# Kernel tuning notes

Measured on AMD Instinct MI355X. Metric: run time of the kernel, lower is better.

## Reference

```python
import jax, jax.numpy as jnp
import numpy as np

N = 50000
NEG_SLOPE = 0.2


def gat_conv(x, src, dst, W, al, ar, b, res=None, activation=None):
    # x: [N, F_in]; W: [F_in, H*D]; al, ar: [H, D]; b: [H*D]
    H, D = al.shape
    h = (x @ W).reshape(-1, H, D)                      # [N, H, D]
    el = jnp.sum(h * al, axis=-1)                      # [N, H]
    er = jnp.sum(h * ar, axis=-1)                      # [N, H]
    e = jax.nn.leaky_relu(el[src] + er[dst], NEG_SLOPE)  # [E, H]
    # edge softmax grouped by destination node
    m = jax.ops.segment_max(e, dst, num_segments=N)    # [N, H]
    ex = jnp.exp(e - m[dst])
    s = jax.ops.segment_sum(ex, dst, num_segments=N)   # [N, H]
    alpha = ex / s[dst]                                # [E, H]
    msg = h[src] * alpha[..., None]                    # [E, H, D]
    out = jax.ops.segment_sum(msg, dst, num_segments=N)  # [N, H, D]
    if res is not None:
        if res is True:  # identity residual (F_in == H*D)
            out = out + x.reshape(-1, H, D)
        else:            # projected residual, res: [F_in, H*D]
            out = out + (x @ res).reshape(-1, H, D)
    out = out + b.reshape(1, H, D)
    if activation is not None:
        out = activation(out)
    return out


def setup_inputs() -> dict:
    key = jax.random.key(0)
    ks = jax.random.split(key, 16)
    E = 800000
    IN, HID, CLS, H = 256, 64, 32, 2
    x = jax.random.normal(ks[0], (N, IN), dtype=jnp.float32)
    edge_src = jax.random.randint(ks[1], (E,), 0, N, dtype=jnp.int32)
    edge_dst = jax.random.randint(ks[2], (E,), 0, N, dtype=jnp.int32)

    def lin(k, fi, fo):
        return jax.random.normal(k, (fi, fo), dtype=jnp.float32) * (1.0 / np.sqrt(fi))

    W0 = lin(ks[3], IN, H * HID)
    al0 = jax.random.normal(ks[4], (H, HID), dtype=jnp.float32) * 0.1
    ar0 = jax.random.normal(ks[5], (H, HID), dtype=jnp.float32) * 0.1
    b0 = jnp.zeros((H * HID,), dtype=jnp.float32)
    W1 = lin(ks[6], H * HID, H * HID)
    al1 = jax.random.normal(ks[7], (H, HID), dtype=jnp.float32) * 0.1
    ar1 = jax.random.normal(ks[8], (H, HID), dtype=jnp.float32) * 0.1
    b1 = jnp.zeros((H * HID,), dtype=jnp.float32)
    W2 = lin(ks[9], H * HID, H * CLS)
    al2 = jax.random.normal(ks[10], (H, CLS), dtype=jnp.float32) * 0.1
    ar2 = jax.random.normal(ks[11], (H, CLS), dtype=jnp.float32) * 0.1
    b2 = jnp.zeros((H * CLS,), dtype=jnp.float32)
    Wres2 = lin(ks[12], H * HID, H * CLS)
    return {"x": x, "edge_src": edge_src, "edge_dst": edge_dst,
            "W0": W0, "al0": al0, "ar0": ar0, "b0": b0,
            "W1": W1, "al1": al1, "ar1": ar1, "b1": b1,
            "W2": W2, "al2": al2, "ar2": ar2, "b2": b2,
            "Wres2": Wres2}


def reference(x, edge_src, edge_dst, W0, al0, ar0, b0, W1, al1, ar1, b1,
              W2, al2, ar2, b2, Wres2):
    elu = jax.nn.elu
    h = gat_conv(x, edge_src, edge_dst, W0, al0, ar0, b0,
                 res=None, activation=elu)
    h = h.reshape(h.shape[0], -1)  # flatten heads: [N, H*D]
    h = gat_conv(h, edge_src, edge_dst, W1, al1, ar1, b1,
                 res=True, activation=elu)  # identity residual
    h = h.reshape(h.shape[0], -1)
    h = gat_conv(h, edge_src, edge_dst, W2, al2, ar2, b2,
                 res=Wres2, activation=None)  # [N, H, CLS]
    logits = h.mean(axis=1)  # mean over heads -> [N, CLS]
    return logits
```

## Files before the change

### kernel.cpp

```cpp
#include <hip/hip_runtime.h>
#include <math.h>


typedef unsigned int uint;
typedef unsigned short ushort;
typedef __attribute__((ext_vector_type(8))) short bf16x8;
typedef __attribute__((ext_vector_type(4))) float f32x4;

#define NBK 196
#define BCAP 4608

__device__ inline uint f2bf(float f) {
    uint u = __float_as_uint(f);
    return (u + 0x7fffu + ((u >> 16) & 1u)) >> 16;
}

__device__ inline uint4 pack8(float4 a, float4 b) {
    return make_uint4(f2bf(a.x) | (f2bf(a.y) << 16), f2bf(a.z) | (f2bf(a.w) << 16),
                      f2bf(b.x) | (f2bf(b.y) << 16), f2bf(b.z) | (f2bf(b.w) << 16));
}

__global__ __launch_bounds__(256) void bucketA_k(
    const int* __restrict__ src, const int* __restrict__ dst, int E,
    int* __restrict__ bcur, uint* __restrict__ bdata) {
    __shared__ int lhist[NBK];
    __shared__ int gbase[NBK];
    const int t = threadIdx.x;
    for (int i = t; i < NBK; i += 256) lhist[i] = 0;
    __syncthreads();
    const int e0 = blockIdx.x * 2048 + t * 8;
    uint payload[8], meta[8];
#pragma unroll
    for (int i = 0; i < 8; ++i) {
        int e = e0 + i;
        if (e < E) {
            int s = src[e], d = dst[e];
            int b = d >> 8;
            int r = atomicAdd(&lhist[b], 1);
            payload[i] = ((uint)s << 8) | (uint)(d & 255);
            meta[i] = ((uint)b << 16) | (uint)r;
        } else {
            meta[i] = 0xffffffffu;
        }
    }
    __syncthreads();
    for (int i = t; i < NBK; i += 256) {
        int c = lhist[i];
        gbase[i] = c ? atomicAdd(&bcur[i], c) : 0;
    }
    __syncthreads();
#pragma unroll
    for (int i = 0; i < 8; ++i) {
        if (meta[i] != 0xffffffffu) {
            int b = meta[i] >> 16;
            int pos = gbase[b] + (int)(meta[i] & 0xffffu);
            if (pos < BCAP) bdata[(size_t)b * BCAP + pos] = payload[i];
        }
    }
}

__global__ __launch_bounds__(256) void bscan_k(const int* __restrict__ bcur,
                                               int* __restrict__ bbase) {
    __shared__ int sm[256];
    int t = threadIdx.x;
    int v = (t < NBK) ? min(bcur[t], BCAP) : 0;
    sm[t] = v;
    __syncthreads();
    for (int o = 1; o < 256; o <<= 1) {
        int add = (t >= o) ? sm[t - o] : 0;
        __syncthreads();
        sm[t] += add;
        __syncthreads();
    }
    if (t < NBK) bbase[t] = sm[t] - v;
}

__global__ __launch_bounds__(256) void bucketB_k(
    const uint* __restrict__ bdata, const int* __restrict__ bcur,
    const int* __restrict__ bbase, int* __restrict__ deg,
    int* __restrict__ offs, int* __restrict__ ssrc, int n) {
    __shared__ int lhist[256], lofs[256], lcur[256], stmp[256];
    const int b = blockIdx.x, t = threadIdx.x;
    const int cnt = min(bcur[b], BCAP);
    const int gb = bbase[b];
    lhist[t] = 0;
    __syncthreads();
    const uint* bd = bdata + (size_t)b * BCAP;
    for (int i = t; i < cnt; i += 256)
        atomicAdd(&lhist[bd[i] & 255], 1);
    __syncthreads();
    int v = lhist[t];
    stmp[t] = v;
    __syncthreads();
    for (int o = 1; o < 256; o <<= 1) {
        int add = (t >= o) ? stmp[t - o] : 0;
        __syncthreads();
        stmp[t] += add;
        __syncthreads();
    }
    lofs[t] = stmp[t] - v;
    lcur[t] = 0;
    __syncthreads();
    int node = b * 256 + t;
    if (node < n) {
        deg[node] = v;
        offs[node] = gb + lofs[t];
    }
    for (int i = t; i < cnt; i += 256) {
        uint p = bd[i];
        int dl = p & 255;
        int r = atomicAdd(&lcur[dl], 1);
        ssrc[gb + lofs[dl] + r] = (int)(p >> 8);
    }
}

__global__ __launch_bounds__(256) void wt_k(
    const float* __restrict__ W0, const float* __restrict__ W1,
    const float* __restrict__ W2, const float* __restrict__ Wr,
    ushort* __restrict__ Wt0, ushort* __restrict__ Wt1,
    ushort* __restrict__ Wt2cat) {
    int b = blockIdx.x, t = threadIdx.x;
    if (b < 128) {
        int i = b * 256 + t;
        int n = i >> 8, k = i & 255;
        Wt0[n * 256 + k] = (ushort)f2bf(W0[k * 128 + n]);
    } else if (b < 192) {
        int i = (b - 128) * 256 + t;
        int n = i >> 7, k = i & 127;
        Wt1[n * 128 + k] = (ushort)f2bf(W1[k * 128 + n]);
    } else if (b < 224) {
        int i = (b - 192) * 256 + t;
        int n = i >> 7, k = i & 127;
        Wt2cat[n * 128 + k] = (ushort)f2bf(W2[k * 64 + n]);
    } else {
        int i = (b - 224) * 256 + t;
        int n = i >> 7, k = i & 127;
        Wt2cat[(64 + n) * 128 + k] = (ushort)f2bf(Wr[k * 64 + n]);
    }
}

template <int K, bool L2MODE, bool AFP32>
__global__ __launch_bounds__(256) void gemm_m(
    const float* __restrict__ Af, const ushort* __restrict__ Ab,
    const ushort* __restrict__ Wt, ushort* __restrict__ Hb,
    float* __restrict__ hres, int nrows,
    const float* __restrict__ al, const float* __restrict__ ar,
    float* __restrict__ el, float* __restrict__ er) {
    constexpr int BK = 64;
    constexpr int AS = 72;
    __shared__ float smem[8448 + 256];
    ushort* As = (ushort*)smem;
    ushort* Ws = (ushort*)smem + 64 * AS;
    float* alr = smem + 8448;
    const int tid = threadIdx.x;
    const int w = tid >> 6;
    const int lane = tid & 63;
    const int l15 = lane & 15, quad = lane >> 4;
    const int row0 = blockIdx.x * 64;
    constexpr int NC = L2MODE ? 64 : 128;

    if (tid < 2 * NC) alr[tid] = (tid < NC) ? al[tid] : ar[tid - NC];

    f32x4 acc[8];
#pragma unroll
    for (int i = 0; i < 8; ++i) acc[i] = (f32x4){0.f, 0.f, 0.f, 0.f};

    for (int kt = 0; kt < K / BK; ++kt) {
        const int k0 = kt * BK;
        if (AFP32) {
#pragma unroll
            for (int t = 0; t < 4; ++t) {
                int idx = tid + t * 256;
                int r = idx >> 4, c4 = idx & 15;
                float4 v = make_float4(0.f, 0.f, 0.f, 0.f);
                if (row0 + r < nrows)
                    v = *(const float4*)&Af[(size_t)(row0 + r) * K + k0 + c4 * 4];
                ushort4 o;
                o.x = (ushort)f2bf(v.x); o.y = (ushort)f2bf(v.y);
                o.z = (ushort)f2bf(v.z); o.w = (ushort)f2bf(v.w);
                *(ushort4*)&As[r * AS + c4 * 4] = o;
            }
        } else {
#pragma unroll
            for (int t = 0; t < 2; ++t) {
                int idx = tid + t * 256;
                int r = idx >> 3, c8 = idx & 7;
                uint4 v = make_uint4(0, 0, 0, 0);
                if (row0 + r < nrows)
                    v = *(const uint4*)&Ab[(size_t)(row0 + r) * K + k0 + c8 * 8];
                *(uint4*)&As[r * AS + c8 * 8] = v;
            }
        }
#pragma unroll
        for (int t = 0; t < 4; ++t) {
            int idx = tid + t * 256;
            int n = idx >> 3, c8 = idx & 7;
            *(uint4*)&Ws[n * AS + c8 * 8] =
                *(const uint4*)&Wt[(size_t)n * K + k0 + c8 * 8];
        }
        __syncthreads();
#pragma unroll
        for (int ks = 0; ks < 2; ++ks) {
            bf16x8 af = *(const bf16x8*)&As[(w * 16 + l15) * AS + ks * 32 + quad * 8];
#pragma unroll
            for (int ct = 0; ct < 8; ++ct) {
                bf16x8 bf = *(const bf16x8*)&Ws[(ct * 16 + l15) * AS + ks * 32 + quad * 8];
                acc[ct] = __builtin_amdgcn_mfma_f32_16x16x32_bf16(af, bf, acc[ct], 0, 0, 0);
            }
        }
        __syncthreads();
    }

    float* Cs = smem;
#pragma unroll
    for (int ct = 0; ct < 8; ++ct)
#pragma unroll
        for (int r = 0; r < 4; ++r)
            Cs[(w * 16 + quad * 4 + r) * 132 + ct * 16 + l15] = acc[ct][r];
    __syncthreads();

    if (L2MODE) {
#pragma unroll
        for (int t = 0; t < 2; ++t) {
            int chunk = tid + t * 256;
            int r = chunk >> 3, c8 = chunk & 7;
            int grow = row0 + r;
            if (grow < nrows) {
                float4 v0 = *(float4*)&Cs[r * 132 + c8 * 8];
                float4 v1 = *(float4*)&Cs[r * 132 + c8 * 8 + 4];
                *(uint4*)&Hb[(size_t)grow * 64 + c8 * 8] = pack8(v0, v1);
            }
        }
#pragma unroll
        for (int t = 0; t < 4; ++t) {
            int chunk = tid + t * 256;
            int r = chunk >> 4, c4 = chunk & 15;
            int grow = row0 + r;
            if (grow < nrows)
                *(float4*)&hres[(size_t)grow * 64 + c4 * 4] =
                    *(float4*)&Cs[r * 132 + 64 + c4 * 4];
        }
    } else {
#pragma unroll
        for (int t = 0; t < 4; ++t) {
            int chunk = tid + t * 256;
            int r = chunk >> 4, c8 = chunk & 15;
            int grow = row0 + r;
            if (grow < nrows) {
                float4 v0 = *(float4*)&Cs[r * 132 + c8 * 8];
                float4 v1 = *(float4*)&Cs[r * 132 + c8 * 8 + 4];
                *(uint4*)&Hb[(size_t)grow * 128 + c8 * 8] = pack8(v0, v1);
            }
        }
    }
    {
        constexpr int HD = L2MODE ? 32 : 64;
        int r = tid >> 2, hh = (tid >> 1) & 1, iser = tid & 1;
        int grow = row0 + r;
        const float* coef = alr + iser * NC + hh * HD;
        const float* crow = Cs + r * 132 + hh * HD;
        float sum = 0.f;
#pragma unroll
        for (int i = 0; i < HD; ++i) sum += crow[i] * coef[i];
        if (grow < nrows) (iser ? er : el)[grow * 2 + hh] = sum;
    }
}

template <int D, bool MEAN_HEADS, bool RES_BF16>
__global__ __launch_bounds__(256) void agg_c(
    const int* __restrict__ ssrc, const int* __restrict__ offs,
    const int* __restrict__ deg, const ushort* __restrict__ hb,
    const float* __restrict__ el, const float* __restrict__ er,
    const float* __restrict__ bias, const void* __restrict__ res,
    float* __restrict__ out, ushort* __restrict__ outb, int act, int n) {
    constexpr int F = 2 * D;
    constexpr int CH = F / 8;
    constexpr int ES = 64 / CH;
    constexpr int UB = 4;
    __shared__ float2 wls_all[4][128];
    const int wid = threadIdx.x >> 6;
    const int lane = threadIdx.x & 63;
    const int node = blockIdx.x * 4 + wid;
    if (node >= n) return;
    float2* wls = wls_all[wid];
    const int off = offs[node];
    const int dg = deg[node];
    const float2 ern = *(const float2*)&er[node * 2];

    float m0, m1, is0, is1;
    const bool small = (dg <= 64);
    if (small) {
        int sidx = 0;
        float a = -INFINITY, b = -INFINITY;
        if (lane < dg) {
            sidx = ssrc[off + lane];
            float2 ev = *(const float2*)&el[sidx * 2];
            a = ev.x + ern.x; a = fmaxf(a, 0.2f * a);
            b = ev.y + ern.y; b = fmaxf(b, 0.2f * b);
        }
        m0 = a; m1 = b;
        for (int o = 32; o; o >>= 1) {
            m0 = fmaxf(m0, __shfl_xor(m0, o));
            m1 = fmaxf(m1, __shfl_xor(m1, o));
        }
        float p0 = (lane < dg) ? __expf(a - m0) : 0.f;
        float p1 = (lane < dg) ? __expf(b - m1) : 0.f;
        float s0 = p0, s1 = p1;
        for (int o = 32; o; o >>= 1) {
            s0 += __shfl_xor(s0, o);
            s1 += __shfl_xor(s1, o);
        }
        is0 = s0 > 0.f ? 1.f / s0 : 0.f;
        is1 = s1 > 0.f ? 1.f / s1 : 0.f;
        wls[lane * 2 + 0] = make_float2(__int_as_float(sidx), p0 * is0);
        wls[lane * 2 + 1] = make_float2(__int_as_float(sidx), p1 * is1);
    } else {
        float s0 = 0.f, s1 = 0.f;
        m0 = -INFINITY; m1 = -INFINITY;
        for (int k = lane; k < dg; k += 64) {
            int sidx = ssrc[off + k];
            float2 ev = *(const float2*)&el[sidx * 2];
            float a = ev.x + ern.x; a = fmaxf(a, 0.2f * a);
            float b = ev.y + ern.y; b = fmaxf(b, 0.2f * b);
            float nm = fmaxf(m0, a);
            s0 = s0 * __expf(m0 - nm) + __expf(a - nm); m0 = nm;
            nm = fmaxf(m1, b);
            s1 = s1 * __expf(m1 - nm) + __expf(b - nm); m1 = nm;
        }
        for (int o = 32; o; o >>= 1) {
            float om = __shfl_xor(m0, o), os = __shfl_xor(s0, o);
            float nm = fmaxf(m0, om);
            s0 = (nm == -INFINITY) ? 0.f : s0 * __expf(m0 - nm) + os * __expf(om - nm);
            m0 = nm;
            om = __shfl_xor(m1, o); os = __shfl_xor(s1, o);
            nm = fmaxf(m1, om);
            s1 = (nm == -INFINITY) ? 0.f : s1 * __expf(m1 - nm) + os * __expf(om - nm);
            m1 = nm;
        }
        is0 = s0 > 0.f ? 1.f / s0 : 0.f;
        is1 = s1 > 0.f ? 1.f / s1 : 0.f;
    }

    const int c = lane & (CH - 1);
    const int es = lane / CH;
    const int h1 = (c >= CH / 2) ? 1 : 0;
    const uint4* __restrict__ hp = (const uint4*)hb;
    const float2* wbase = wls + es * 2 + h1;
    float acc[8];
#pragma unroll
    for (int i = 0; i < 8; ++i) acc[i] = 0.f;

    for (int c0 = 0; c0 < dg; c0 += 64) {
        if (!small) {
            int k = c0 + lane;
            int sidx = 0;
            float w0 = 0.f, w1 = 0.f;
            if (k < dg) {
                sidx = ssrc[off + k];
                float2 ev = *(const float2*)&el[sidx * 2];
                float a = ev.x + ern.x; a = fmaxf(a, 0.2f * a);
                float b = ev.y + ern.y; b = fmaxf(b, 0.2f * b);
                w0 = __expf(a - m0) * is0;
                w1 = __expf(b - m1) * is1;
            }
            wls[lane * 2 + 0] = make_float2(__int_as_float(sidx), w0);
            wls[lane * 2 + 1] = make_float2(__int_as_float(sidx), w1);
        }
        const int cnt = min(64, dg - c0);
        for (int p = 0; p < cnt; p += UB * ES) {
            float2 mw[UB];
#pragma unroll
            for (int u = 0; u < UB; ++u)
                mw[u] = wbase[(p + u * ES) * 2];
            uint4 q[UB];
#pragma unroll
            for (int u = 0; u < UB; ++u)
                q[u] = hp[(size_t)__float_as_int(mw[u].x) * CH + c];
#pragma unroll
            for (int u = 0; u < UB; ++u) {
                float wj = mw[u].y;
                acc[0] += wj * __uint_as_float(q[u].x << 16);
                acc[1] += wj * __uint_as_float(q[u].x & 0xffff0000u);
                acc[2] += wj * __uint_as_float(q[u].y << 16);
                acc[3] += wj * __uint_as_float(q[u].y & 0xffff0000u);
                acc[4] += wj * __uint_as_float(q[u].z << 16);
                acc[5] += wj * __uint_as_float(q[u].z & 0xffff0000u);
                acc[6] += wj * __uint_as_float(q[u].w << 16);
                acc[7] += wj * __uint_as_float(q[u].w & 0xffff0000u);
            }
        }
    }

#pragma unroll
    for (int o = CH; o < 64; o <<= 1) {
#pragma unroll
        for (int i = 0; i < 8; ++i) acc[i] += __shfl_xor(acc[i], o);
    }

    const int f0 = c * 8;
    float4 b0v = *(const float4*)&bias[f0];
    float4 b1v = *(const float4*)&bias[f0 + 4];
    float vv[8] = {acc[0] + b0v.x, acc[1] + b0v.y, acc[2] + b0v.z, acc[3] + b0v.w,
                   acc[4] + b1v.x, acc[5] + b1v.y, acc[6] + b1v.z, acc[7] + b1v.w};
    if (res) {
        if (RES_BF16) {
            uint4 r = ((const uint4*)res)[(size_t)node * CH + c];
            vv[0] += __uint_as_float(r.x << 16);
            vv[1] += __uint_as_float(r.x & 0xffff0000u);
            vv[2] += __uint_as_float(r.y << 16);
            vv[3] += __uint_as_float(r.y & 0xffff0000u);
            vv[4] += __uint_as_float(r.z << 16);
            vv[5] += __uint_as_float(r.z & 0xffff0000u);
            vv[6] += __uint_as_float(r.w << 16);
            vv[7] += __uint_as_float(r.w & 0xffff0000u);
        } else {
            const float* rf = (const float*)res;
            float4 r0v = *(const float4*)&rf[(size_t)node * F + f0];
            float4 r1v = *(const float4*)&rf[(size_t)node * F + f0 + 4];
            vv[0] += r0v.x; vv[1] += r0v.y; vv[2] += r0v.z; vv[3] += r0v.w;
            vv[4] += r1v.x; vv[5] += r1v.y; vv[6] += r1v.z; vv[7] += r1v.w;
        }
    }
    if (act) {
#pragma unroll
        for (int i = 0; i < 8; ++i)
            vv[i] = vv[i] > 0.f ? vv[i] : __expf(vv[i]) - 1.f;
    }
    if (MEAN_HEADS) {
        float ov[8];
#pragma unroll
        for (int i = 0; i < 8; ++i) ov[i] = __shfl_xor(vv[i], CH / 2);
        if (es == 0 && c < CH / 2) {
            float4 u0 = make_float4(0.5f * (vv[0] + ov[0]), 0.5f * (vv[1] + ov[1]),
                                    0.5f * (vv[2] + ov[2]), 0.5f * (vv[3] + ov[3]));
            float4 u1 = make_float4(0.5f * (vv[4] + ov[4]), 0.5f * (vv[5] + ov[5]),
                                    0.5f * (vv[6] + ov[6]), 0.5f * (vv[7] + ov[7]));
            *(float4*)&out[(size_t)node * D + f0] = u0;
            *(float4*)&out[(size_t)node * D + f0 + 4] = u1;
        }
    } else if (es == 0) {
        if (out) {
            *(float4*)&out[(size_t)node * F + f0] =
                make_float4(vv[0], vv[1], vv[2], vv[3]);
            *(float4*)&out[(size_t)node * F + f0 + 4] =
                make_float4(vv[4], vv[5], vv[6], vv[7]);
        }
        if (outb) {
            *(uint4*)&outb[(size_t)node * F + f0] =
                pack8(make_float4(vv[0], vv[1], vv[2], vv[3]),
                      make_float4(vv[4], vv[5], vv[6], vv[7]));
        }
    }
}


extern "C" void kernel_launch(void* const* d_in, const int* in_sizes, int n_in,
                              void* d_out, int out_size, void* d_ws, size_t ws_size,
                              hipStream_t stream) {
    const float* x     = (const float*)d_in[0];
    const int*   esrc  = (const int*)d_in[1];
    const int*   edst  = (const int*)d_in[2];
    const float* W0    = (const float*)d_in[3];
    const float* al0   = (const float*)d_in[4];
    const float* ar0   = (const float*)d_in[5];
    const float* b0    = (const float*)d_in[6];
    const float* W1    = (const float*)d_in[7];
    const float* al1   = (const float*)d_in[8];
    const float* ar1   = (const float*)d_in[9];
    const float* b1    = (const float*)d_in[10];
    const float* W2    = (const float*)d_in[11];
    const float* al2   = (const float*)d_in[12];
    const float* ar2   = (const float*)d_in[13];
    const float* b2    = (const float*)d_in[14];
    const float* Wres2 = (const float*)d_in[15];

    const int N = in_sizes[0] / 256;
    const int E = in_sizes[1];

    float* ws = (float*)d_ws;
    float* hres  = ws;
    float* el    = hres + (size_t)N * 64;
    float* er    = el + (size_t)N * 2;
    int* deg     = (int*)(er + (size_t)N * 2);
    int* offs    = deg + N;
    int* bcur    = offs + N;
    int* bbase   = bcur + 256;
    int* ssrc    = bbase + 256;
    uint* bdata  = (uint*)(ssrc + E);
    ushort* Hb   = (ushort*)(bdata + (size_t)NBK * BCAP);
    ushort* Ab   = Hb + (size_t)N * 128;
    ushort* Bb   = Ab + (size_t)N * 128;
    ushort* Wt0  = Bb + (size_t)N * 128;
    ushort* Wt1  = Wt0 + 128 * 256;
    ushort* Wt2c = Wt1 + 128 * 128;

    hipMemsetAsync(bcur, 0, NBK * sizeof(int), stream);
    bucketA_k<<<(E + 2047) / 2048, 256, 0, stream>>>(esrc, edst, E, bcur, bdata);
    bscan_k<<<1, 256, 0, stream>>>(bcur, bbase);
    bucketB_k<<<NBK, 256, 0, stream>>>(bdata, bcur, bbase, deg, offs, ssrc, N);

    wt_k<<<256, 256, 0, stream>>>(W0, W1, W2, Wres2, Wt0, Wt1, Wt2c);

    int gblk = (N + 63) / 64;
    int ablk = (N + 3) / 4;

    gemm_m<256, false, true><<<gblk, 256, 0, stream>>>(
        x, nullptr, Wt0, Hb, nullptr, N, al0, ar0, el, er);
    agg_c<64, false, false><<<ablk, 256, 0, stream>>>(
        ssrc, offs, deg, Hb, el, er, b0, nullptr, nullptr, Ab, 1, N);

    gemm_m<128, false, false><<<gblk, 256, 0, stream>>>(
        nullptr, Ab, Wt1, Hb, nullptr, N, al1, ar1, el, er);
    agg_c<64, false, true><<<ablk, 256, 0, stream>>>(
        ssrc, offs, deg, Hb, el, er, b1, Ab, nullptr, Bb, 1, N);

    gemm_m<128, true, false><<<gblk, 256, 0, stream>>>(
        nullptr, Bb, Wt2c, Hb, hres, N, al2, ar2, el, er);
    agg_c<32, true, false><<<ablk, 256, 0, stream>>>(
        ssrc, offs, deg, Hb, el, er, b2, hres, (float*)d_out, nullptr, 0, N);
}
```

Before: 305.0 us.

## Bin nodes by degree and pack several low-degree nodes per wavefront

Adds a binning pass that sorts nodes into three degree classes (≤16, ≤32, >32) and a persistent aggregation kernel that processes 4, 2 or 1 nodes per 64-lane wavefront depending on class. With average degree around 16, most wavefronts previously left many lanes idle during the softmax and gather phases. The cost is two extra small kernels, a memset, and indirection through node lists, which also change the output write order. The node lists reuse the bucket scratch buffer, which is no longer needed at that point.

```diff
diff --git a/kernel.cpp b/kernel.cpp
--- a/kernel.cpp
+++ b/kernel.cpp
@@ -112,6 +112,37 @@
         int r = atomicAdd(&lcur[dl], 1);
         ssrc[gb + lofs[dl] + r] = (int)(p >> 8);
     }
+}
+
+__global__ __launch_bounds__(256) void bin_k(
+    const int* __restrict__ deg, int n, int* __restrict__ nl0,
+    int* __restrict__ nl1, int* __restrict__ nl2, int* __restrict__ cnt) {
+    __shared__ int lc[3], lb[3];
+    const int t = threadIdx.x;
+    if (t < 3) lc[t] = 0;
+    __syncthreads();
+    int node = blockIdx.x * 256 + t;
+    int cls = -1, r = 0;
+    if (node < n) {
+        int d = deg[node];
+        cls = (d <= 16) ? 0 : ((d <= 32) ? 1 : 2);
+        r = atomicAdd(&lc[cls], 1);
+    }
+    __syncthreads();
+    if (t < 3) lb[t] = lc[t] ? atomicAdd(&cnt[t], lc[t]) : 0;
+    __syncthreads();
+    if (node < n) {
+        int* nl = (cls == 0) ? nl0 : ((cls == 1) ? nl1 : nl2);
+        nl[lb[cls] + r] = node;
+    }
+}
+
+__global__ void sched_k(int* __restrict__ meta) {
+    int I0 = (meta[0] + 3) >> 2;
+    int I1 = (meta[1] + 1) >> 1;
+    meta[3] = I0;
+    meta[4] = I0 + I1;
+    meta[5] = I0 + I1 + meta[2];
 }
 
 __global__ __launch_bounds__(256) void wt_k(
@@ -266,112 +297,43 @@
     }
 }
 
-template <int D, bool MEAN_HEADS, bool RES_BF16>
-__global__ __launch_bounds__(256) void agg_c(
+template <int D, bool MEAN_HEADS, bool RES_BF16, int LPN>
+__device__ __forceinline__ void agg_group(
+    int node, int lane, float2* __restrict__ wlsw,
     const int* __restrict__ ssrc, const int* __restrict__ offs,
     const int* __restrict__ deg, const ushort* __restrict__ hb,
     const float* __restrict__ el, const float* __restrict__ er,
     const float* __restrict__ bias, const void* __restrict__ res,
-    float* __restrict__ out, ushort* __restrict__ outb, int act, int n) {
+    float* __restrict__ out, ushort* __restrict__ outb, int act) {
     constexpr int F = 2 * D;
     constexpr int CH = F / 8;
-    constexpr int ES = 64 / CH;
+    constexpr int ESL = LPN / CH;
     constexpr int UB = 4;
-    __shared__ float2 wls_all[4][128];
-    const int wid = threadIdx.x >> 6;
-    const int lane = threadIdx.x & 63;
-    const int node = blockIdx.x * 4 + wid;
-    if (node >= n) return;
-    float2* wls = wls_all[wid];
-    const int off = offs[node];
-    const int dg = deg[node];
-    const float2 ern = *(const float2*)&er[node * 2];
-
-    float m0, m1, is0, is1;
-    const bool small = (dg <= 64);
-    if (small) {
-        int sidx = 0;
-        float a = -INFINITY, b = -INFINITY;
-        if (lane < dg) {
-            sidx = ssrc[off + lane];
-            float2 ev = *(const float2*)&el[sidx * 2];
-            a = ev.x + ern.x; a = fmaxf(a, 0.2f * a);
-            b = ev.y + ern.y; b = fmaxf(b, 0.2f * b);
-        }
-        m0 = a; m1 = b;
-        for (int o = 32; o; o >>= 1) {
-            m0 = fmaxf(m0, __shfl_xor(m0, o));
-            m1 = fmaxf(m1, __shfl_xor(m1, o));
-        }
-        float p0 = (lane < dg) ? __expf(a - m0) : 0.f;
-        float p1 = (lane < dg) ? __expf(b - m1) : 0.f;
-        float s0 = p0, s1 = p1;
-        for (int o = 32; o; o >>= 1) {
-            s0 += __shfl_xor(s0, o);
-            s1 += __shfl_xor(s1, o);
-        }
-        is0 = s0 > 0.f ? 1.f / s0 : 0.f;
-        is1 = s1 > 0.f ? 1.f / s1 : 0.f;
-        wls[lane * 2 + 0] = make_float2(__int_as_float(sidx), p0 * is0);
-        wls[lane * 2 + 1] = make_float2(__int_as_float(sidx), p1 * is1);
-    } else {
-        float s0 = 0.f, s1 = 0.f;
-        m0 = -INFINITY; m1 = -INFINITY;
-        for (int k = lane; k < dg; k += 64) {
-            int sidx = ssrc[off + k];
-            float2 ev = *(const float2*)&el[sidx * 2];
-            float a = ev.x + ern.x; a = fmaxf(a, 0.2f * a);
-            float b = ev.y + ern.y; b = fmaxf(b, 0.2f * b);
-            float nm = fmaxf(m0, a);
-            s0 = s0 * __expf(m0 - nm) + __expf(a - nm); m0 = nm;
-            nm = fmaxf(m1, b);
-            s1 = s1 * __expf(m1 - nm) + __expf(b - nm); m1 = nm;
-        }
-        for (int o = 32; o; o >>= 1) {
-            float om = __shfl_xor(m0, o), os = __shfl_xor(s0, o);
-            float nm = fmaxf(m0, om);
-            s0 = (nm == -INFINITY) ? 0.f : s0 * __expf(m0 - nm) + os * __expf(om - nm);
-            m0 = nm;
-            om = __shfl_xor(m1, o); os = __shfl_xor(s1, o);
-            nm = fmaxf(m1, om);
-            s1 = (nm == -INFINITY) ? 0.f : s1 * __expf(m1 - nm) + os * __expf(om - nm);
-            m1 = nm;
-        }
-        is0 = s0 > 0.f ? 1.f / s0 : 0.f;
-        is1 = s1 > 0.f ? 1.f / s1 : 0.f;
-    }
-
-    const int c = lane & (CH - 1);
-    const int es = lane / CH;
+    static_assert(ESL >= 1, "LPN must cover a full row");
+    const int g = lane / LPN, sl = lane % LPN;
+    const bool valid = node >= 0;
+    float2* wls = wlsw + g * (LPN * 2);
+    int off = 0, dg = 0;
+    float2 ern = make_float2(0.f, 0.f);
+    if (valid) {
+        off = offs[node];
+        dg = deg[node];
+        ern = *(const float2*)&er[node * 2];
+    }
+    const uint4* __restrict__ hp = (const uint4*)hb;
+    const int c = sl & (CH - 1);
+    const int es = sl / CH;
     const int h1 = (c >= CH / 2) ? 1 : 0;
-    const uint4* __restrict__ hp = (const uint4*)hb;
     const float2* wbase = wls + es * 2 + h1;
     float acc[8];
 #pragma unroll
     for (int i = 0; i < 8; ++i) acc[i] = 0.f;
 
-    for (int c0 = 0; c0 < dg; c0 += 64) {
-        if (!small) {
-            int k = c0 + lane;
-            int sidx = 0;
-            float w0 = 0.f, w1 = 0.f;
-            if (k < dg) {
-                sidx = ssrc[off + k];
-                float2 ev = *(const float2*)&el[sidx * 2];
-                float a = ev.x + ern.x; a = fmaxf(a, 0.2f * a);
-                float b = ev.y + ern.y; b = fmaxf(b, 0.2f * b);
-                w0 = __expf(a - m0) * is0;
-                w1 = __expf(b - m1) * is1;
-            }
-            wls[lane * 2 + 0] = make_float2(__int_as_float(sidx), w0);
-            wls[lane * 2 + 1] = make_float2(__int_as_float(sidx), w1);
-        }
-        const int cnt = min(64, dg - c0);
-        for (int p = 0; p < cnt; p += UB * ES) {
+    auto inner = [&](int cnt) {
+        for (int p = 0; p < cnt; p += UB * ESL) {
             float2 mw[UB];
 #pragma unroll
-            for (int u = 0; u < UB; ++u)
-                mw[u] = wbase[(p + u * ES) * 2];
+            for (int u = 0; u < UB; ++u) mw[u] = wbase[(p + u * ESL) * 2];
             uint4 q[UB];
 #pragma unroll
             for (int u = 0; u < UB; ++u)
@@ -389,13 +351,88 @@
                 acc[7] += wj * __uint_as_float(q[u].w & 0xffff0000u);
             }
         }
-    }
-
-#pragma unroll
-    for (int o = CH; o < 64; o <<= 1) {
+    };
+
+    bool big = false;
+    if constexpr (LPN == 64) big = (dg > 64);
+
+    if (!big) {
+        int sidx = 0;
+        float a = -INFINITY, b = -INFINITY;
+        if (valid && sl < dg) {
+            sidx = ssrc[off + sl];
+            float2 ev = *(const float2*)&el[sidx * 2];
+            a = ev.x + ern.x; a = fmaxf(a, 0.2f * a);
+            b = ev.y + ern.y; b = fmaxf(b, 0.2f * b);
+        }
+        float m0 = a, m1 = b;
+#pragma unroll
+        for (int o = LPN / 2; o; o >>= 1) {
+            m0 = fmaxf(m0, __shfl_xor(m0, o));
+            m1 = fmaxf(m1, __shfl_xor(m1, o));
+        }
+        float p0 = (valid && sl < dg) ? __expf(a - m0) : 0.f;
+        float p1 = (valid && sl < dg) ? __expf(b - m1) : 0.f;
+        float s0 = p0, s1 = p1;
+#pragma unroll
+        for (int o = LPN / 2; o; o >>= 1) {
+            s0 += __shfl_xor(s0, o);
+            s1 += __shfl_xor(s1, o);
+        }
+        float is0 = s0 > 0.f ? 1.f / s0 : 0.f;
+        float is1 = s1 > 0.f ? 1.f / s1 : 0.f;
+        wls[sl * 2 + 0] = make_float2(__int_as_float(sidx), p0 * is0);
+        wls[sl * 2 + 1] = make_float2(__int_as_float(sidx), p1 * is1);
+        inner(dg);
+    } else if constexpr (LPN == 64) {
+        float s0 = 0.f, s1 = 0.f;
+        float m0 = -INFINITY, m1 = -INFINITY;
+        for (int k = sl; k < dg; k += 64) {
+            int sidx = ssrc[off + k];
+            float2 ev = *(const float2*)&el[sidx * 2];
+            float a = ev.x + ern.x; a = fmaxf(a, 0.2f * a);
+            float b = ev.y + ern.y; b = fmaxf(b, 0.2f * b);
+            float nm = fmaxf(m0, a);
+            s0 = s0 * __expf(m0 - nm) + __expf(a - nm); m0 = nm;
+            nm = fmaxf(m1, b);
+            s1 = s1 * __expf(m1 - nm) + __expf(b - nm); m1 = nm;
+        }
+        for (int o = 32; o; o >>= 1) {
+            float om = __shfl_xor(m0, o), os = __shfl_xor(s0, o);
+            float nm = fmaxf(m0, om);
+            s0 = (nm == -INFINITY) ? 0.f : s0 * __expf(m0 - nm) + os * __expf(om - nm);
+            m0 = nm;
+            om = __shfl_xor(m1, o); os = __shfl_xor(s1, o);
+            nm = fmaxf(m1, om);
+            s1 = (nm == -INFINITY) ? 0.f : s1 * __expf(m1 - nm) + os * __expf(om - nm);
+            m1 = nm;
+        }
+        float is0 = s0 > 0.f ? 1.f / s0 : 0.f;
+        float is1 = s1 > 0.f ? 1.f / s1 : 0.f;
+        for (int cc = 0; cc < dg; cc += 64) {
+            int k = cc + sl;
+            int sidx = 0;
+            float w0 = 0.f, w1 = 0.f;
+            if (k < dg) {
+                sidx = ssrc[off + k];
+                float2 ev = *(const float2*)&el[sidx * 2];
+                float a = ev.x + ern.x; a = fmaxf(a, 0.2f * a);
+                float b = ev.y + ern.y; b = fmaxf(b, 0.2f * b);
+                w0 = __expf(a - m0) * is0;
+                w1 = __expf(b - m1) * is1;
+            }
+            wls[sl * 2 + 0] = make_float2(__int_as_float(sidx), w0);
+            wls[sl * 2 + 1] = make_float2(__int_as_float(sidx), w1);
+            inner(min(64, dg - cc));
+        }
+    }
+
+#pragma unroll
+    for (int o = CH; o < LPN; o <<= 1) {
 #pragma unroll
         for (int i = 0; i < 8; ++i) acc[i] += __shfl_xor(acc[i], o);
     }
+    if (!valid) return;
 
     const int f0 = c * 8;
     float4 b0v = *(const float4*)&bias[f0];
@@ -453,6 +490,44 @@
     }
 }
 
+template <int D, bool MEAN_HEADS, bool RES_BF16>
+__global__ __launch_bounds__(256) void agg_c2(
+    const int* __restrict__ meta, const int* __restrict__ nl0,
+    const int* __restrict__ nl1, const int* __restrict__ nl2,
+    const int* __restrict__ ssrc, const int* __restrict__ offs,
+    const int* __restrict__ deg, const ushort* __restrict__ hb,
+    const float* __restrict__ el, const float* __restrict__ er,
+    const float* __restrict__ bias, const void* __restrict__ res,
+    float* __restrict__ out, ushort* __restrict__ outb, int act) {
+    __shared__ float2 wls_all[4][128];
+    const int wid = threadIdx.x >> 6;
+    const int lane = threadIdx.x & 63;
+    float2* wls = wls_all[wid];
+    const int c0 = meta[0], c1 = meta[1];
+    const int I0 = meta[3], I01 = meta[4], T = meta[5];
+    const int nW = gridDim.x * 4;
+    for (int it = blockIdx.x * 4 + wid; it < T; it += nW) {
+        if (it < I0) {
+            int idx = it * 4 + (lane >> 4);
+            int node = (idx < c0) ? nl0[idx] : -1;
+            agg_group<D, MEAN_HEADS, RES_BF16, 16>(node, lane, wls, ssrc, offs,
+                                                   deg, hb, el, er, bias, res,
+                                                   out, outb, act);
+        } else if (it < I01) {
+            int idx = (it - I0) * 2 + (lane >> 5);
+            int node = (idx < c1) ? nl1[idx] : -1;
+            agg_group<D, MEAN_HEADS, RES_BF16, 32>(node, lane, wls, ssrc, offs,
+                                                   deg, hb, el, er, bias, res,
+                                                   out, outb, act);
+        } else {
+            int node = nl2[it - I01];
+            agg_group<D, MEAN_HEADS, RES_BF16, 64>(node, lane, wls, ssrc, offs,
+                                                   deg, hb, el, er, bias, res,
+                                                   out, outb, act);
+        }
+    }
+}
+
 
 extern "C" void kernel_launch(void* const* d_in, const int* in_sizes, int n_in,
                               void* d_out, int out_size, void* d_ws, size_t ws_size,
@@ -494,28 +569,40 @@
     ushort* Wt1  = Wt0 + 128 * 256;
     ushort* Wt2c = Wt1 + 128 * 128;
 
+    int* meta = (int*)bdata;
+    int* nl0  = meta + 16;
+    int* nl1  = nl0 + N;
+    int* nl2  = nl1 + N;
+
     hipMemsetAsync(bcur, 0, NBK * sizeof(int), stream);
     bucketA_k<<<(E + 2047) / 2048, 256, 0, stream>>>(esrc, edst, E, bcur, bdata);
     bscan_k<<<1, 256, 0, stream>>>(bcur, bbase);
     bucketB_k<<<NBK, 256, 0, stream>>>(bdata, bcur, bbase, deg, offs, ssrc, N);
 
+    hipMemsetAsync(meta, 0, 6 * sizeof(int), stream);
+    bin_k<<<(N + 255) / 256, 256, 0, stream>>>(deg, N, nl0, nl1, nl2, meta);
+    sched_k<<<1, 1, 0, stream>>>(meta);
+
     wt_k<<<256, 256, 0, stream>>>(W0, W1, W2, Wres2, Wt0, Wt1, Wt2c);
 
     int gblk = (N + 63) / 64;
-    int ablk = (N + 3) / 4;
+    const int ablk = 2048;
 
     gemm_m<256, false, true><<<gblk, 256, 0, stream>>>(
         x, nullptr, Wt0, Hb, nullptr, N, al0, ar0, el, er);
-    agg_c<64, false, false><<<ablk, 256, 0, stream>>>(
-        ssrc, offs, deg, Hb, el, er, b0, nullptr, nullptr, Ab, 1, N);
+    agg_c2<64, false, false><<<ablk, 256, 0, stream>>>(
+        meta, nl0, nl1, nl2, ssrc, offs, deg, Hb, el, er, b0, nullptr,
+        nullptr, Ab, 1);
 
     gemm_m<128, false, false><<<gblk, 256, 0, stream>>>(
         nullptr, Ab, Wt1, Hb, nullptr, N, al1, ar1, el, er);
-    agg_c<64, false, true><<<ablk, 256, 0, stream>>>(
-        ssrc, offs, deg, Hb, el, er, b1, Ab, nullptr, Bb, 1, N);
+    agg_c2<64, false, true><<<ablk, 256, 0, stream>>>(
+        meta, nl0, nl1, nl2, ssrc, offs, deg, Hb, el, er, b1, Ab,
+        nullptr, Bb, 1);
 
     gemm_m<128, true, false><<<gblk, 256, 0, stream>>>(
         nullptr, Bb, Wt2c, Hb, hres, N, al2, ar2, el, er);
-    agg_c<32, true, false><<<ablk, 256, 0, stream>>>(
-        ssrc, offs, deg, Hb, el, er, b2, hres, (float*)d_out, nullptr, 0, N);
-}
+    agg_c2<32, true, false><<<ablk, 256, 0, stream>>>(
+        meta, nl0, nl1, nl2, ssrc, offs, deg, Hb, el, er, b2, hres,
+        (float*)d_out, nullptr, 0);
+}
```

Result: faster. 287.5 us (-5.7%).
